# Performance work log

Measured on AMD Instinct MI355X. Metric: run time of the kernel, lower is better.

## Reference

```python
import jax, jax.numpy as jnp
import numpy as np

B, L, D, H, NE, M = 4, 1024, 768, 12, 42, 8
P = NE * (NE - 1)
OFFSET = 1  # BERT [CLS] offset, matching self.offset = 1
EPS = 1e-5


def setup_inputs() -> dict:
    key = jax.random.key(0)
    k1, k2, k3, k4 = jax.random.split(key, 4)
    sequence_output = jax.random.normal(k1, (B, L, D), dtype=jnp.float32)
    # post-softmax attention probs are nonnegative
    attention = jax.random.uniform(k2, (B, H, L, L), dtype=jnp.float32)
    mention_pos = jax.random.randint(k3, (B, NE, M), 0, L - 2)
    mask = (jax.random.uniform(k4, (B, NE, M)) < 0.5).astype(jnp.float32)
    mention_mask = mask.at[:, :, 0].set(1.0)  # every entity has >= 1 mention
    # hts: all ordered entity pairs (h != t), same for every doc
    ii, jj = jnp.meshgrid(jnp.arange(NE), jnp.arange(NE), indexing='ij')
    pairs = jnp.stack([ii.ravel(), jj.ravel()], axis=-1)
    pairs = pairs[np.asarray(ii.ravel() != jj.ravel())]  # [P, 2]
    hts = jnp.broadcast_to(pairs[None], (B, P, 2)).astype(jnp.int64)
    return dict(sequence_output=sequence_output, attention=attention,
                mention_mask=mention_mask,
                mention_pos=mention_pos.astype(jnp.int64), hts=hts)


def reference(sequence_output, attention, mention_mask, mention_pos, hts):
    idx = mention_pos + OFFSET  # [B, NE, M], all < L by construction

    # --- get_entity_embed: gather mention-start token embeds, masked logsumexp over mentions ---
    m_emb = jax.vmap(lambda so, i: so[i])(sequence_output, idx)  # [B, NE, M, D]
    neg = jnp.finfo(m_emb.dtype).min
    entity_embed = jax.nn.logsumexp(
        jnp.where(mention_mask[..., None] > 0, m_emb, neg), axis=2)  # [B, NE, D]

    # --- get_hrt: gather attention rows at mention starts, masked mean over mentions ---
    m_att = jax.vmap(lambda att, i: att[:, i])(attention, idx)  # [B, H, NE, M, L]
    mm = mention_mask[:, None, :, :, None]                      # [B, 1, NE, M, 1]
    entity_att = (m_att * mm).sum(3) / mm.sum(3)                # [B, H, NE, L]

    # --- get_channel_map: all-pairs head*tail attention, mean over heads, normalize, contract ---
    ht_att = jnp.einsum('bhil,bhjl->bijl', entity_att, entity_att) / H  # [B, NE, NE, L]
    ht_att = ht_att / (ht_att.sum(-1, keepdims=True) + EPS)
    feature_map = jnp.einsum('bijl,bld->bijd', ht_att, sequence_output)  # [B, NE, NE, D]

    # --- get_ht: gather per-pair features ---
    h_t = jax.vmap(lambda fm, ht: fm[ht[:, 0], ht[:, 1]])(feature_map, hts)  # [B, P, D]
    return entity_embed, h_t.reshape(B * P, D)
```

## Files before the change

### kernel.cpp

```cpp
#include <hip/hip_runtime.h>
#include <hip/hip_bf16.h>
#include <math.h>

constexpr int Bn  = 4;
constexpr int Ln  = 1024;
constexpr int Dn  = 768;
constexpr int Hn  = 12;
constexpr int NEn = 42;
constexpr int Mn  = 8;
constexpr int Pn  = NEn * (NEn - 1);
constexpr int OFFn = 1;
constexpr float EPSn = 1e-5f;
constexpr int CL = 32;
constexpr int CHUNKS = Ln / CL;
constexpr int QP = 432;

constexpr int SOT_BLKS = (Ln / 64) * (Dn / 32) * Bn;
constexpr int EA_BLKS  = Bn * Hn * NEn;

typedef __attribute__((ext_vector_type(8))) short bf16x8;
typedef __attribute__((ext_vector_type(4))) float f32x4;

__device__ inline unsigned short f2bf(float v) {
    unsigned u = __float_as_uint(v);
    u += 0x7fffu + ((u >> 16) & 1u);
    return (unsigned short)(u >> 16);
}

__device__ inline void gld16(const unsigned short* g, unsigned short* l) {
    typedef __attribute__((address_space(3))) unsigned lds_u32;
    typedef const __attribute__((address_space(1))) unsigned glb_u32;
    __builtin_amdgcn_global_load_lds((glb_u32*)g, (lds_u32*)(uintptr_t)l, 16, 0, 0);
}

__global__ __launch_bounds__(256) void k_entity_embed(
    const float* __restrict__ so, const float* __restrict__ mask,
    const int* __restrict__ mpos, float* __restrict__ out)
{
    const int be = blockIdx.x;
    const int b = be / NEn, e = be % NEn;
    __shared__ int   s_idx[Mn];
    __shared__ float s_msk[Mn];
    if (threadIdx.x < Mn) {
        const int m = threadIdx.x;
        s_idx[m] = mpos[(b * NEn + e) * Mn + m] + OFFn;
        s_msk[m] = mask[(b * NEn + e) * Mn + m];
    }
    __syncthreads();
    for (int d = threadIdx.x; d < Dn; d += 256) {
        float v[Mn];
        float mx = -3.4e38f;
        #pragma unroll
        for (int m = 0; m < Mn; ++m) {
            const float val = so[((size_t)b * Ln + s_idx[m]) * Dn + d];
            v[m] = (s_msk[m] > 0.f) ? val : -3.4e38f;
            mx = fmaxf(mx, v[m]);
        }
        float s = 0.f;
        #pragma unroll
        for (int m = 0; m < Mn; ++m)
            s += (v[m] > -3.0e38f) ? __expf(v[m] - mx) : 0.f;
        out[((size_t)b * NEn + e) * Dn + d] = mx + __logf(s);
    }
}

__global__ __launch_bounds__(256) void k_prep(
    const float* __restrict__ so, const float* __restrict__ att,
    const float* __restrict__ mask, const int* __restrict__ mpos,
    unsigned short* __restrict__ soT, unsigned short* __restrict__ ea2)
{
    const int bx = blockIdx.x;
    if (bx < SOT_BLKS) {
        __shared__ unsigned short tile[64][33];
        constexpr int tilesPerB = (Ln / 64) * (Dn / 32);
        const int rem = bx % tilesPerB;
        const int b   = bx / tilesPerB;
        const int l0  = (rem % (Ln / 64)) * 64;
        const int d0  = (rem / (Ln / 64)) * 32;
        const int cx = threadIdx.x & 31;
        const int ry = threadIdx.x >> 5;
        for (int r = ry; r < 64; r += 8)
            tile[r][cx] = f2bf(so[((size_t)b * Ln + l0 + r) * Dn + d0 + cx]);
        __syncthreads();
        for (int r = ry; r < 32; r += 8) {
            const unsigned v = (unsigned)tile[2 * cx][r] |
                               ((unsigned)tile[2 * cx + 1][r] << 16);
            *(unsigned*)&soT[((size_t)b * Dn + d0 + r) * Ln + l0 + 2 * cx] = v;
        }
    } else {
        const int id = bx - SOT_BLKS;
        const int e = id % NEn;
        const int bh = id / NEn;
        const int h = bh % Hn;
        const int b = bh / Hn;
        __shared__ int   s_idx[Mn];
        __shared__ float s_w[Mn];
        __shared__ float s_inv;
        if (threadIdx.x == 0) {
            float sum = 0.f;
            for (int m = 0; m < Mn; ++m) {
                s_idx[m] = mpos[(b * NEn + e) * Mn + m] + OFFn;
                const float w = mask[(b * NEn + e) * Mn + m];
                s_w[m] = w; sum += w;
            }
            s_inv = 1.f / sum;
        }
        __syncthreads();
        const int l = threadIdx.x * 4;
        float4 acc = {0.f, 0.f, 0.f, 0.f};
        #pragma unroll
        for (int m = 0; m < Mn; ++m) {
            if (s_w[m] > 0.f) {
                const float4 v = *(const float4*)&att[(((size_t)b * Hn + h) * Ln + s_idx[m]) * Ln + l];
                acc.x += v.x; acc.y += v.y; acc.z += v.z; acc.w += v.w;
            }
        }
        const unsigned u0 = (unsigned)f2bf(acc.x * s_inv) | ((unsigned)f2bf(acc.y * s_inv) << 16);
        const unsigned u1 = (unsigned)f2bf(acc.z * s_inv) | ((unsigned)f2bf(acc.w * s_inv) << 16);
        uint2 uu; uu.x = u0; uu.y = u1;
        *(uint2*)&ea2[((size_t)id) * Ln + l] = uu;
    }
}

__global__ __launch_bounds__(256) void k_pairs(
    const unsigned short* __restrict__ ea2, unsigned short* __restrict__ xb,
    float* __restrict__ Spart)
{
    __shared__ unsigned sm[Hn * NEn * 17];
    const int c    = blockIdx.x;
    const int q    = blockIdx.y;
    const int b    = blockIdx.z;
    const int t    = threadIdx.x;

    const unsigned* eg = (const unsigned*)ea2 + ((size_t)b * Hn * NEn) * (Ln / 2) + c * (CL / 2);
    for (int id = t; id < Hn * NEn * 16; id += 256) {
        const int r = id >> 4, u = id & 15;
        sm[r * 17 + u] = eg[(size_t)r * (Ln / 2) + u];
    }
    __syncthreads();

    const int l2 = t & 15;
    const int pm = t >> 4;
    const int rend = min((q + 1) * QP, Pn);
    unsigned* xbu = (unsigned*)xb;
    for (int rk = q * QP + pm; rk < rend; rk += 16) {
        const int i  = rk / (NEn - 1);
        const int jj = rk % (NEn - 1);
        const int j  = jj + (jj >= i ? 1 : 0);
        float a0 = 0.f, a1 = 0.f;
        #pragma unroll
        for (int h = 0; h < Hn; ++h) {
            const unsigned ui = sm[(h * NEn + i) * 17 + l2];
            const unsigned uj = sm[(h * NEn + j) * 17 + l2];
            const float xi0 = __uint_as_float(ui << 16);
            const float xi1 = __uint_as_float(ui & 0xffff0000u);
            const float xj0 = __uint_as_float(uj << 16);
            const float xj1 = __uint_as_float(uj & 0xffff0000u);
            a0 = fmaf(xi0, xj0, a0);
            a1 = fmaf(xi1, xj1, a1);
        }
        xbu[((size_t)b * Pn + rk) * (Ln / 2) + c * (CL / 2) + l2] =
            (unsigned)f2bf(a0) | ((unsigned)f2bf(a1) << 16);
        float part = a0 + a1;
        part += __shfl_down(part, 8, 16);
        part += __shfl_down(part, 4, 16);
        part += __shfl_down(part, 2, 16);
        part += __shfl_down(part, 1, 16);
        if (l2 == 0)
            Spart[((size_t)b * CHUNKS + c) * Pn + rk] = part;
    }
}

__global__ __launch_bounds__(256) void k_gemm_mfma(
    const unsigned short* __restrict__ xb, const unsigned short* __restrict__ soT,
    const float* __restrict__ Spart, float* __restrict__ out2)
{
    __shared__ __align__(16) unsigned short As[2][64 * 32];
    __shared__ __align__(16) unsigned short Bs[2][128 * 32];
    __shared__ float s_scale[64];

    constexpr int nbx = (Pn + 63) / 64;
    constexpr int nby = Dn / 128;
    constexpr int nwg = nbx * nby * Bn;
    int bid = (int)blockIdx.x;
    bid = (bid & 7) * (nwg >> 3) + (bid >> 3);
    const int b    = bid / (nbx * nby);
    const int rem  = bid % (nbx * nby);
    const int row0 = (rem % nbx) * 64;
    const int col0 = (rem / nbx) * 128;

    const int t    = threadIdx.x;
    const int lane = t & 63;
    const int wave = t >> 6;
    const int wm = wave & 1, wn = wave >> 1;

    if (t < 64) {
        const int r = min(row0 + t, Pn - 1);
        float s = 0.f;
        #pragma unroll
        for (int cix = 0; cix < CHUNKS; ++cix)
            s += Spart[((size_t)b * CHUNKS + cix) * Pn + r];
        s_scale[t] = 1.0f / (s + (float)Hn * EPSn);
    }

    f32x4 acc[2][4];
    #pragma unroll
    for (int i2 = 0; i2 < 2; ++i2)
        #pragma unroll
        for (int j2 = 0; j2 < 4; ++j2)
            acc[i2][j2] = (f32x4){0.f, 0.f, 0.f, 0.f};

    const int rq = t >> 2;
    const int cq = t & 3;
    const int sw0 = (cq ^ ((rq >> 1) & 3)) * 8;
    const int sw1 = (cq ^ (((rq + 64) >> 1) & 3)) * 8;
    const unsigned short* gA  = xb  + ((size_t)b * Pn + min(row0 + rq, Pn - 1)) * Ln + sw0;
    const unsigned short* gB0 = soT + ((size_t)b * Dn + col0 + rq) * Ln + sw0;
    const unsigned short* gB1 = soT + ((size_t)b * Dn + col0 + rq + 64) * Ln + sw1;
    const int ldsOffA  = (wave << 6) * 8;
    const int ldsOffB0 = (wave << 6) * 8;
    const int ldsOffB1 = 2048 + (wave << 6) * 8;

    const int fr   = lane & 15;
    const int koq  = lane >> 4;
    const int coff = (koq ^ ((fr >> 1) & 3)) * 8;

    gld16(gA,  &As[0][ldsOffA]);
    gld16(gB0, &Bs[0][ldsOffB0]);
    gld16(gB1, &Bs[0][ldsOffB1]);
    __syncthreads();

    for (int k0 = 0; k0 < 32; ++k0) {
        const int cur = k0 & 1;
        if (k0 < 31) {
            const int koff = (k0 + 1) * 32;
            const int nxt = cur ^ 1;
            gld16(gA  + koff, &As[nxt][ldsOffA]);
            gld16(gB0 + koff, &Bs[nxt][ldsOffB0]);
            gld16(gB1 + koff, &Bs[nxt][ldsOffB1]);
        }

        bf16x8 af[2], bfr[4];
        #pragma unroll
        for (int mt = 0; mt < 2; ++mt)
            af[mt] = *(const bf16x8*)&As[cur][(wm * 32 + mt * 16 + fr) * 32 + coff];
        #pragma unroll
        for (int nt = 0; nt < 4; ++nt)
            bfr[nt] = *(const bf16x8*)&Bs[cur][(wn * 64 + nt * 16 + fr) * 32 + coff];
        #pragma unroll
        for (int mt = 0; mt < 2; ++mt)
            #pragma unroll
            for (int nt = 0; nt < 4; ++nt)
                acc[mt][nt] = __builtin_amdgcn_mfma_f32_16x16x32_bf16(
                    af[mt], bfr[nt], acc[mt][nt], 0, 0, 0);

        __syncthreads();
    }

    const int ccol  = lane & 15;
    const int crow4 = (lane >> 4) * 4;
    #pragma unroll
    for (int mt = 0; mt < 2; ++mt) {
        #pragma unroll
        for (int rg = 0; rg < 4; ++rg) {
            const int ml = wm * 32 + mt * 16 + crow4 + rg;
            const int r  = row0 + ml;
            if (r < Pn) {
                const float sc2 = s_scale[ml];
                float* dst = out2 + ((size_t)b * Pn + r) * Dn + col0 + wn * 64 + ccol;
                #pragma unroll
                for (int nt = 0; nt < 4; ++nt)
                    dst[nt * 16] = acc[mt][nt][rg] * sc2;
            }
        }
    }
}

extern "C" void kernel_launch(void* const* d_in, const int* in_sizes, int n_in,
                              void* d_out, int out_size, void* d_ws, size_t ws_size,
                              hipStream_t stream)
{
    const float* so   = (const float*)d_in[0];
    const float* att  = (const float*)d_in[1];
    const float* mask = (const float*)d_in[2];
    const int*   mpos = (const int*)d_in[3];
    float* out = (float*)d_out;
    float* out_ee = out;
    float* out_ht = out + (size_t)Bn * NEn * Dn;

    char* w = (char*)d_ws;
    unsigned short* ea2 = (unsigned short*)w; w += (size_t)Bn * Hn * NEn * Ln * 2;
    unsigned short* xb  = (unsigned short*)w; w += (size_t)Bn * Pn * Ln * 2;
    unsigned short* soT = (unsigned short*)w; w += (size_t)Bn * Dn * Ln * 2;
    float* Spart = (float*)w;

    hipLaunchKernelGGL(k_prep, dim3(SOT_BLKS + EA_BLKS), dim3(256), 0, stream,
                       so, att, mask, mpos, soT, ea2);
    hipLaunchKernelGGL(k_pairs, dim3(CHUNKS, 4, Bn), dim3(256), 0, stream,
                       ea2, xb, Spart);
    hipLaunchKernelGGL(k_gemm_mfma, dim3(((Pn + 63) / 64) * (Dn / 128) * Bn), dim3(256), 0, stream,
                       xb, soT, Spart, out_ht);
    hipLaunchKernelGGL(k_entity_embed, dim3(Bn * NEn), dim3(256), 0, stream,
                       so, mask, mpos, out_ee);
}
```

Before: 305.2 us.

## Use 32x32x16 MFMA in GEMM, reuse head-entity regs in pairs, vectorize entity embed

The GEMM switches from 16x16x32 to 32x32x16 bf16 MFMA tiles with matching swizzled LDS fragment loads and a new output mapping, so each wave issues fewer, larger matrix instructions. The pairs kernel now walks entity i in groups of 7 (6 groups), holds i's per-head values in registers and loops over j, which removes the repeated LDS reads of i. The entity-embed kernel uses 192 threads with float4 loads and stores, and skips loads for masked mentions. The combined changes alter register pressure and the store pattern; the 32x32 epilogue writes scalar floats per row.

After: 302.1 us. No clear change (-1.0%).

```diff
diff --git a/kernel.cpp b/kernel.cpp
--- a/kernel.cpp
+++ b/kernel.cpp
@@ -13,13 +13,13 @@
 constexpr float EPSn = 1e-5f;
 constexpr int CL = 32;
 constexpr int CHUNKS = Ln / CL;
-constexpr int QP = 432;
 
 constexpr int SOT_BLKS = (Ln / 64) * (Dn / 32) * Bn;
 constexpr int EA_BLKS  = Bn * Hn * NEn;
 
 typedef __attribute__((ext_vector_type(8))) short bf16x8;
 typedef __attribute__((ext_vector_type(4))) float f32x4;
+typedef __attribute__((ext_vector_type(16))) float f32x16;
 
 __device__ inline unsigned short f2bf(float v) {
     unsigned u = __float_as_uint(v);
@@ -33,7 +33,7 @@
     __builtin_amdgcn_global_load_lds((glb_u32*)g, (lds_u32*)(uintptr_t)l, 16, 0, 0);
 }
 
-__global__ __launch_bounds__(256) void k_entity_embed(
+__global__ __launch_bounds__(192) void k_entity_embed(
     const float* __restrict__ so, const float* __restrict__ mask,
     const int* __restrict__ mpos, float* __restrict__ out)
 {
@@ -47,21 +47,31 @@
         s_msk[m] = mask[(b * NEn + e) * Mn + m];
     }
     __syncthreads();
-    for (int d = threadIdx.x; d < Dn; d += 256) {
-        float v[Mn];
+    const int t = threadIdx.x;
+    float v[4][Mn];
+    #pragma unroll
+    for (int m = 0; m < Mn; ++m) {
+        if (s_msk[m] > 0.f) {
+            const float4 t4 = *(const float4*)&so[((size_t)b * Ln + s_idx[m]) * Dn + 4 * t];
+            v[0][m] = t4.x; v[1][m] = t4.y; v[2][m] = t4.z; v[3][m] = t4.w;
+        } else {
+            v[0][m] = v[1][m] = v[2][m] = v[3][m] = -3.4e38f;
+        }
+    }
+    float4 res;
+    float* rp = (float*)&res;
+    #pragma unroll
+    for (int c = 0; c < 4; ++c) {
         float mx = -3.4e38f;
         #pragma unroll
-        for (int m = 0; m < Mn; ++m) {
-            const float val = so[((size_t)b * Ln + s_idx[m]) * Dn + d];
-            v[m] = (s_msk[m] > 0.f) ? val : -3.4e38f;
-            mx = fmaxf(mx, v[m]);
-        }
+        for (int m = 0; m < Mn; ++m) mx = fmaxf(mx, v[c][m]);
         float s = 0.f;
         #pragma unroll
         for (int m = 0; m < Mn; ++m)
-            s += (v[m] > -3.0e38f) ? __expf(v[m] - mx) : 0.f;
-        out[((size_t)b * NEn + e) * Dn + d] = mx + __logf(s);
-    }
+            s += (v[c][m] > -3.0e38f) ? __expf(v[c][m] - mx) : 0.f;
+        rp[c] = mx + __logf(s);
+    }
+    *(float4*)&out[((size_t)b * NEn + e) * Dn + 4 * t] = res;
 }
 
 __global__ __launch_bounds__(256) void k_prep(
@@ -128,7 +138,7 @@
 {
     __shared__ unsigned sm[Hn * NEn * 17];
     const int c    = blockIdx.x;
-    const int q    = blockIdx.y;
+    const int g    = blockIdx.y;
     const int b    = blockIdx.z;
     const int t    = threadIdx.x;
 
@@ -141,33 +151,36 @@
 
     const int l2 = t & 15;
     const int pm = t >> 4;
-    const int rend = min((q + 1) * QP, Pn);
     unsigned* xbu = (unsigned*)xb;
-    for (int rk = q * QP + pm; rk < rend; rk += 16) {
-        const int i  = rk / (NEn - 1);
-        const int jj = rk % (NEn - 1);
-        const int j  = jj + (jj >= i ? 1 : 0);
-        float a0 = 0.f, a1 = 0.f;
+
+    for (int i = g * 7; i < g * 7 + 7; ++i) {
+        float xi0[Hn], xi1[Hn];
         #pragma unroll
         for (int h = 0; h < Hn; ++h) {
             const unsigned ui = sm[(h * NEn + i) * 17 + l2];
-            const unsigned uj = sm[(h * NEn + j) * 17 + l2];
-            const float xi0 = __uint_as_float(ui << 16);
-            const float xi1 = __uint_as_float(ui & 0xffff0000u);
-            const float xj0 = __uint_as_float(uj << 16);
-            const float xj1 = __uint_as_float(uj & 0xffff0000u);
-            a0 = fmaf(xi0, xj0, a0);
-            a1 = fmaf(xi1, xj1, a1);
-        }
-        xbu[((size_t)b * Pn + rk) * (Ln / 2) + c * (CL / 2) + l2] =
-            (unsigned)f2bf(a0) | ((unsigned)f2bf(a1) << 16);
-        float part = a0 + a1;
-        part += __shfl_down(part, 8, 16);
-        part += __shfl_down(part, 4, 16);
-        part += __shfl_down(part, 2, 16);
-        part += __shfl_down(part, 1, 16);
-        if (l2 == 0)
-            Spart[((size_t)b * CHUNKS + c) * Pn + rk] = part;
+            xi0[h] = __uint_as_float(ui << 16);
+            xi1[h] = __uint_as_float(ui & 0xffff0000u);
+        }
+        for (int jj = pm; jj < NEn - 1; jj += 16) {
+            const int j = jj + (jj >= i ? 1 : 0);
+            float a0 = 0.f, a1 = 0.f;
+            #pragma unroll
+            for (int h = 0; h < Hn; ++h) {
+                const unsigned uj = sm[(h * NEn + j) * 17 + l2];
+                a0 = fmaf(xi0[h], __uint_as_float(uj << 16), a0);
+                a1 = fmaf(xi1[h], __uint_as_float(uj & 0xffff0000u), a1);
+            }
+            const int rk = i * (NEn - 1) + jj;
+            xbu[((size_t)b * Pn + rk) * (Ln / 2) + c * (CL / 2) + l2] =
+                (unsigned)f2bf(a0) | ((unsigned)f2bf(a1) << 16);
+            float part = a0 + a1;
+            part += __shfl_down(part, 8, 16);
+            part += __shfl_down(part, 4, 16);
+            part += __shfl_down(part, 2, 16);
+            part += __shfl_down(part, 1, 16);
+            if (l2 == 0)
+                Spart[((size_t)b * CHUNKS + c) * Pn + rk] = part;
+        }
     }
 }
 
@@ -203,12 +216,12 @@
         s_scale[t] = 1.0f / (s + (float)Hn * EPSn);
     }
 
-    f32x4 acc[2][4];
+    f32x16 acc[2];
     #pragma unroll
-    for (int i2 = 0; i2 < 2; ++i2)
-        #pragma unroll
-        for (int j2 = 0; j2 < 4; ++j2)
-            acc[i2][j2] = (f32x4){0.f, 0.f, 0.f, 0.f};
+    for (int nt = 0; nt < 2; ++nt)
+        #pragma unroll
+        for (int rg = 0; rg < 16; ++rg)
+            acc[nt][rg] = 0.f;
 
     const int rq = t >> 2;
     const int cq = t & 3;
@@ -221,9 +234,14 @@
     const int ldsOffB0 = (wave << 6) * 8;
     const int ldsOffB1 = 2048 + (wave << 6) * 8;
 
-    const int fr   = lane & 15;
-    const int koq  = lane >> 4;
-    const int coff = (koq ^ ((fr >> 1) & 3)) * 8;
+    const int lr = lane & 31;
+    const int kh = lane >> 5;
+    const int rowA = wm * 32 + lr;
+    const int keyA = (rowA >> 1) & 3;
+    const int rowB0 = wn * 64 + lr;
+    const int rowB1 = wn * 64 + 32 + lr;
+    const int keyB0 = (rowB0 >> 1) & 3;
+    const int keyB1 = (rowB1 >> 1) & 3;
 
     gld16(gA,  &As[0][ldsOffA]);
     gld16(gB0, &Bs[0][ldsOffB0]);
@@ -240,37 +258,32 @@
             gld16(gB1 + koff, &Bs[nxt][ldsOffB1]);
         }
 
-        bf16x8 af[2], bfr[4];
-        #pragma unroll
-        for (int mt = 0; mt < 2; ++mt)
-            af[mt] = *(const bf16x8*)&As[cur][(wm * 32 + mt * 16 + fr) * 32 + coff];
-        #pragma unroll
-        for (int nt = 0; nt < 4; ++nt)
-            bfr[nt] = *(const bf16x8*)&Bs[cur][(wn * 64 + nt * 16 + fr) * 32 + coff];
-        #pragma unroll
-        for (int mt = 0; mt < 2; ++mt)
-            #pragma unroll
-            for (int nt = 0; nt < 4; ++nt)
-                acc[mt][nt] = __builtin_amdgcn_mfma_f32_16x16x32_bf16(
-                    af[mt], bfr[nt], acc[mt][nt], 0, 0, 0);
+        bf16x8 af[2], bf0[2], bf1[2];
+        #pragma unroll
+        for (int s = 0; s < 2; ++s) {
+            const int cc = s * 2 + kh;
+            af[s]  = *(const bf16x8*)&As[cur][rowA  * 32 + ((cc ^ keyA)  * 8)];
+            bf0[s] = *(const bf16x8*)&Bs[cur][rowB0 * 32 + ((cc ^ keyB0) * 8)];
+            bf1[s] = *(const bf16x8*)&Bs[cur][rowB1 * 32 + ((cc ^ keyB1) * 8)];
+        }
+        #pragma unroll
+        for (int s = 0; s < 2; ++s) {
+            acc[0] = __builtin_amdgcn_mfma_f32_32x32x16_bf16(af[s], bf0[s], acc[0], 0, 0, 0);
+            acc[1] = __builtin_amdgcn_mfma_f32_32x32x16_bf16(af[s], bf1[s], acc[1], 0, 0, 0);
+        }
 
         __syncthreads();
     }
 
-    const int ccol  = lane & 15;
-    const int crow4 = (lane >> 4) * 4;
     #pragma unroll
-    for (int mt = 0; mt < 2; ++mt) {
-        #pragma unroll
-        for (int rg = 0; rg < 4; ++rg) {
-            const int ml = wm * 32 + mt * 16 + crow4 + rg;
+    for (int nt = 0; nt < 2; ++nt) {
+        #pragma unroll
+        for (int rg = 0; rg < 16; ++rg) {
+            const int ml = wm * 32 + (rg & 3) + 8 * (rg >> 2) + 4 * kh;
             const int r  = row0 + ml;
             if (r < Pn) {
-                const float sc2 = s_scale[ml];
-                float* dst = out2 + ((size_t)b * Pn + r) * Dn + col0 + wn * 64 + ccol;
-                #pragma unroll
-                for (int nt = 0; nt < 4; ++nt)
-                    dst[nt * 16] = acc[mt][nt][rg] * sc2;
+                out2[((size_t)b * Pn + r) * Dn + col0 + wn * 64 + nt * 32 + lr] =
+                    acc[nt][rg] * s_scale[ml];
             }
         }
     }
@@ -296,10 +309,10 @@
 
     hipLaunchKernelGGL(k_prep, dim3(SOT_BLKS + EA_BLKS), dim3(256), 0, stream,
                        so, att, mask, mpos, soT, ea2);
-    hipLaunchKernelGGL(k_pairs, dim3(CHUNKS, 4, Bn), dim3(256), 0, stream,
+    hipLaunchKernelGGL(k_pairs, dim3(CHUNKS, 6, Bn), dim3(256), 0, stream,
                        ea2, xb, Spart);
     hipLaunchKernelGGL(k_gemm_mfma, dim3(((Pn + 63) / 64) * (Dn / 128) * Bn), dim3(256), 0, stream,
                        xb, soT, Spart, out_ht);
-    hipLaunchKernelGGL(k_entity_embed, dim3(Bn * NEn), dim3(256), 0, stream,
+    hipLaunchKernelGGL(k_entity_embed, dim3(Bn * NEn), dim3(192), 0, stream,
                        so, mask, mpos, out_ee);
 }
```
